# Kernel tuning notes

Measured on AMD Instinct MI355X. Metric: run time of the kernel, lower is better.

The kernel has to match this reference:

```python
import jax, jax.numpy as jnp
import numpy as np


def _icosa_group():
    """60 rotation matrices of the icosahedral rotation group (vertex anchors)."""
    phi = (1.0 + 5.0 ** 0.5) / 2.0

    def rot(axis, ang):
        a = np.asarray(axis, dtype=np.float64)
        a = a / np.linalg.norm(a)
        K = np.array([[0.0, -a[2], a[1]], [a[2], 0.0, -a[0]], [-a[1], a[0], 0.0]])
        return np.eye(3) + np.sin(ang) * K + (1.0 - np.cos(ang)) * (K @ K)

    # two distinct 5-fold vertex axes generate the full group of order 60
    gens = [rot([0.0, 1.0, phi], 2.0 * np.pi / 5.0),
            rot([0.0, -1.0, phi], 2.0 * np.pi / 5.0)]
    mats = {tuple(np.round(np.eye(3), 6).ravel()): np.eye(3)}
    frontier = [np.eye(3)]
    while frontier:
        new = []
        for m in frontier:
            for g in gens:
                p = g @ m
                k = tuple(np.round(p, 6).ravel())
                if k not in mats:
                    mats[k] = p
                    new.append(p)
        frontier = new
    Rs = np.stack([mats[k] for k in sorted(mats.keys())]).astype(np.float32)
    assert Rs.shape[0] == 60
    return Rs


def _normalize(x, axis=-1, eps=1e-12):
    n = jnp.linalg.norm(x, axis=axis, keepdims=True)
    return x / jnp.maximum(n, eps)


def setup_inputs() -> dict:
    key = jax.random.key(0)
    ks = jax.random.split(key, 6)
    bs, P, N = 2, 1024, 16
    d_in, d_out, K = 64, 32, 7
    neighbor_index = jax.random.randint(ks[0], (bs, P, N), 0, P, dtype=jnp.int32)
    vertices = jax.random.normal(ks[1], (bs, P, 3), dtype=jnp.float32)
    feature_map = jax.random.normal(ks[2], (bs, d_in, P, 3), dtype=jnp.float32)
    W = jax.random.normal(ks[3], (d_out, d_in, K, 3), dtype=jnp.float32) * (2.0 / (d_in * K * 3 + d_out * K * 3)) ** 0.5
    W_center = jax.random.normal(ks[4], (d_out, d_in), dtype=jnp.float32) * (2.0 / (d_in + d_out)) ** 0.5
    directions = jax.random.normal(ks[5], (d_out, K, 3), dtype=jnp.float32) * (2.0 / (d_out * 3 + K * 3)) ** 0.5
    Rs = jnp.asarray(_icosa_group())
    return {"neighbor_index": neighbor_index, "vertices": vertices,
            "feature_map": feature_map, "W": W, "W_center": W_center,
            "directions": directions, "Rs": Rs}


def reference(neighbor_index, vertices, feature_map, W, W_center, directions, Rs):
    bs, P, N = neighbor_index.shape
    d_out, d_in, K, _ = W.shape
    n_bin = 5
    interval = Rs.shape[0] // n_bin

    # neighbor direction unit vectors [b,p,n,3]
    nbrs = jax.vmap(lambda v_b, i_b: v_b[i_b])(vertices, neighbor_index)
    ndn = _normalize(nbrs - vertices[:, :, None, :])
    kd = _normalize(directions)  # [d,k,3]

    # ---- stage 1: rotation search (fully detached in the torch original) ----
    ndn_s = jax.lax.stop_gradient(ndn)
    kd_s = jax.lax.stop_gradient(kd)
    W_s = jax.lax.stop_gradient(W)
    fm_s = jax.lax.stop_gradient(feature_map)
    Rs_s = jax.lax.stop_gradient(Rs)

    r_vals, r_idxs = [], []
    for i in range(n_bin):
        Rsi = Rs_s[i * interval:(i + 1) * interval]  # [r,3,3]
        kd_ro = jnp.einsum('dkj,rij->dkir', kd_s, Rsi)          # [d,k,3,r]
        theta = jnp.einsum('dkjr,bpnj->bdkpnr', kd_ro, ndn_s)   # [b,d,k,p,n,r]
        W_ro = jnp.einsum('dckj,rij->dckir', W_s, Rsi)          # [d,c,k,3,r]
        fo = jnp.einsum('dckir,bcpi->bdkpr', W_ro, fm_s)        # [b,d,k,p,r]
        gathered = jax.vmap(lambda f_b, i_b: f_b[:, :, i_b, :])(fo, neighbor_index)  # [b,d,k,p,n,r]
        ka = gathered * theta
        ka = jnp.max(ka, axis=4)   # max over neighbors -> [b,d,k,p,r]
        ka = jnp.sum(ka, axis=2)   # sum over kernel pts -> [b,d,p,r]
        r_vals.append(jnp.max(ka, axis=-1))
        r_idxs.append(jnp.argmax(ka, axis=-1) + i * interval)
    r_vals = jnp.stack(r_vals, axis=-1)  # [b,d,p,5]
    r_idxs = jnp.stack(r_idxs, axis=-1)  # [b,d,p,5]
    best_bin = jnp.argmax(r_vals, axis=-1)  # [b,d,p]
    r_index = jnp.take_along_axis(r_idxs, best_bin[..., None], axis=-1)[..., 0]  # [b,d,p]
    match_R = Rs[r_index]  # [b,d,p,3,3]

    # ---- stage 2: apply best rotation (differentiable) ----
    kd_ro2 = jnp.einsum('dkj,bdpij->bdkpi', kd, match_R)               # [b,d,k,p,3]
    theta2 = jax.nn.relu(jnp.einsum('bdkpj,bpnj->bdkpn', kd_ro2, ndn))  # [b,d,k,p,n]
    fo2 = jnp.einsum('dckj,bdpij,bcpi->bdkp', W, match_R, feature_map)  # [b,d,k,p]
    gathered2 = jax.vmap(lambda f_b, i_b: f_b[:, :, i_b])(fo2, neighbor_index)  # [b,d,k,p,n]
    ka2 = gathered2 * theta2
    kaw2 = jnp.max(ka2, axis=4)  # [b,d,k,p]
    out = jnp.einsum('bdkp,bdkpi->bdpi', kaw2, kd_ro2)
    center = jnp.einsum('dc,bcpi->bdpi', W_center, feature_map)
    return out + center
```

## Files before the change

kernel.cpp:

```cpp
#include <hip/hip_runtime.h>
#include <math.h>

#define BS   2
#define PP   1024
#define NN   16
#define CIN  64
#define DOUT 32
#define KK   7
#define NR   60
#define NT2  30

#define OFF_NDN  0
#define OFF_KROT 98304
#define OFF_M    138624
#define OFF_PVAL 4332928
#define OFF_PIDX 6299008
#define OFF_FO2  6790528
#define OFF_RIDX 7314816

#define NEG_INF (-3.402823466e38f)

typedef float v2f __attribute__((ext_vector_type(2)));
typedef float v4f __attribute__((ext_vector_type(4)));

__device__ __forceinline__ float sload(const float* __restrict__ p, int idx) {
    return __int_as_float(__builtin_amdgcn_readfirstlane(__float_as_int(p[idx])));
}

__device__ __forceinline__ v2f pk_mul_sv(v2f s, v2f v) {
    v2f d; asm("v_pk_mul_f32 %0, %1, %2" : "=v"(d) : "s"(s), "v"(v)); return d;
}
__device__ __forceinline__ v2f pk_fma_svv(v2f s, v2f v, v2f c) {
    v2f d; asm("v_pk_fma_f32 %0, %1, %2, %3" : "=v"(d) : "s"(s), "v"(v), "v"(c)); return d;
}
__device__ __forceinline__ v2f pk_mul_vv(v2f a, v2f b) {
    v2f d; asm("v_pk_mul_f32 %0, %1, %2" : "=v"(d) : "v"(a), "v"(b)); return d;
}

__device__ __forceinline__ float quad_max(float x) {
    float y = __int_as_float(__builtin_amdgcn_mov_dpp(
        __float_as_int(x), 0xB1, 0xF, 0xF, true));
    x = fmaxf(x, y);
    float z = __int_as_float(__builtin_amdgcn_mov_dpp(
        __float_as_int(x), 0x4E, 0xF, 0xF, true));
    return fmaxf(x, z);
}

__global__ __launch_bounds__(256) void k_pre(const int* __restrict__ nbr,
                                             const float* __restrict__ vert,
                                             const float* __restrict__ dirs,
                                             const float* __restrict__ Rs,
                                             float* __restrict__ ws) {
    int tid = blockIdx.x * 256 + threadIdx.x;
    if (tid < BS * PP * NN) {
        int p = (tid >> 4) & (PP - 1);
        int b = tid >> 14;
        int q = nbr[tid];
        const float* vp = vert + ((b << 10) + p) * 3;
        const float* vq = vert + ((b << 10) + q) * 3;
        float dx = vq[0] - vp[0], dy = vq[1] - vp[1], dz = vq[2] - vp[2];
        float nrm = sqrtf(dx * dx + dy * dy + dz * dz);
        float den = fmaxf(nrm, 1e-12f);
        dx /= den; dy /= den; dz /= den;
        float* o = ws + OFF_NDN + tid * 3;
        o[0] = dx; o[1] = dy; o[2] = dz;
    }
    int t2 = tid - BS * PP * NN;
    if (t2 >= 0 && t2 < DOUT * NR * KK) {
        int k = t2 % KK;
        int r = (t2 / KK) % NR;
        int d = t2 / (KK * NR);
        const float* dk = dirs + (d * KK + k) * 3;
        float x = dk[0], y = dk[1], z = dk[2];
        float nrm = sqrtf(x * x + y * y + z * z);
        float den = fmaxf(nrm, 1e-12f);
        x /= den; y /= den; z /= den;
        const float* R = Rs + r * 9;
        float* o = ws + OFF_KROT + t2 * 3;
        o[0] = R[0] * x + R[1] * y + R[2] * z;
        o[1] = R[3] * x + R[4] * y + R[5] * z;
        o[2] = R[6] * x + R[7] * y + R[8] * z;
    }
}

__global__ __launch_bounds__(256, 2) void k_buildM(const float* __restrict__ fm,
                                                   const float* __restrict__ W,
                                                   float* __restrict__ Mout) {
    int d = blockIdx.y, b = blockIdx.z;
    int p = blockIdx.x * 256 + threadIdx.x;

    float M[64];
#pragma unroll
    for (int t = 0; t < 64; t++) M[t] = 0.f;

    const float* fbase = fm + (size_t)(b * CIN * PP + p) * 3;
    const float* wbase = W + (size_t)d * CIN * KK * 3;
    for (int c = 0; c < CIN; c++) {
        const float* f = fbase + c * PP * 3;
        float f0 = f[0], f1 = f[1], f2 = f[2];
        const float* wl = wbase + c * 21;
#pragma unroll
        for (int k = 0; k < KK; k++) {
#pragma unroll
            for (int j = 0; j < 3; j++) {
                float w = sload(wl, k * 3 + j);
                M[k * 9 + 0 + j] += w * f0;
                M[k * 9 + 3 + j] += w * f1;
                M[k * 9 + 6 + j] += w * f2;
            }
        }
    }
    float4* o = (float4*)(Mout + (size_t)(((b * DOUT + d) << 10) + p) * 64);
#pragma unroll
    for (int t = 0; t < 15; t++)
        o[t] = make_float4(M[4 * t], M[4 * t + 1], M[4 * t + 2], M[4 * t + 3]);
    o[15] = make_float4(M[60], M[61], M[62], 0.f);
}

__device__ __forceinline__ int fo_base(int p) {
    return (p << 2) ^ ((p >> 1) & 7);
}

__global__ __launch_bounds__(1024)
void k_score(const int* __restrict__ nbr,
             const float* __restrict__ Rs,
             const float* __restrict__ Mptr,
             const float* __restrict__ ndn,
             const float* __restrict__ krot,
             float* __restrict__ pval,
             unsigned char* __restrict__ pidx8) {
    __shared__ v4f fo4s[PP * 4];
    const int tile = blockIdx.x, d = blockIdx.y, b = blockIdx.z;
    const int bd = b * DOUT + d;
    const int rbase = tile * 2;
    const int tq = threadIdx.x >> 2;
    const int ns = threadIdx.x & 3;

    {
        const int p = threadIdx.x;
        float Rc0[9], Rc1[9];
#pragma unroll
        for (int j = 0; j < 9; j++) {
            Rc0[j] = sload(Rs, (rbase + 0) * 9 + j);
            Rc1[j] = sload(Rs, (rbase + 1) * 9 + j);
        }
        float fo0[KK], fo1[KK];
#pragma unroll
        for (int k = 0; k < KK; k++) { fo0[k] = 0.f; fo1[k] = 0.f; }

        const float4* m4 = (const float4*)(Mptr + (size_t)((bd << 10) + p) * 64);
#pragma unroll
        for (int t = 0; t < 16; t++) {
            float4 v = m4[t];
            float e[4] = {v.x, v.y, v.z, v.w};
#pragma unroll
            for (int ee = 0; ee < 4; ee++) {
                const int g = 4 * t + ee;
                if (g < 63) {
                    const int k = g / 9, r9 = g % 9;
                    fo0[k] += Rc0[r9] * e[ee];
                    fo1[k] += Rc1[r9] * e[ee];
                }
            }
            if ((t & 3) == 3)
                __builtin_amdgcn_sched_barrier(0);
        }
        const int fb = fo_base(p);
        v4f s0; s0.x = fo0[0]; s0.y = fo1[0]; s0.z = fo0[1]; s0.w = fo1[1];
        v4f s1; s1.x = fo0[2]; s1.y = fo1[2]; s1.z = fo0[3]; s1.w = fo1[3];
        v4f s2; s2.x = fo0[4]; s2.y = fo1[4]; s2.z = fo0[5]; s2.w = fo1[5];
        v4f s3; s3.x = fo0[6]; s3.y = fo1[6]; s3.z = 0.f;    s3.w = 0.f;
        fo4s[fb]     = s0;
        fo4s[fb ^ 1] = s1;
        fo4s[fb ^ 2] = s2;
        fo4s[fb ^ 3] = s3;
    }
    __syncthreads();

    v2f vkp[KK][3];
    {
        const int kb0 = (d * NR + rbase + 0) * 21;
        const int kb1 = (d * NR + rbase + 1) * 21;
#pragma unroll
        for (int k = 0; k < KK; k++)
#pragma unroll
            for (int c = 0; c < 3; c++) {
                v2f t; t.x = sload(krot, kb0 + k * 3 + c);
                       t.y = sload(krot, kb1 + k * 3 + c);
                vkp[k][c] = t;
            }
    }
    const v2f* fo2s = (const v2f*)fo4s;

#pragma unroll
    for (int pp = 0; pp < 4; pp++) {
        const int p2 = (pp << 8) + tq;

        int4 nv = *(const int4*)(nbr + (((size_t)((b << 10) + p2)) << 4) + (ns << 2));
        float u[12];
        {
            const float4* u4 = (const float4*)(ndn + ((size_t)((b << 10) + p2) * 16 + (ns << 2)) * 3);
            float4 a = u4[0], bb = u4[1], cc = u4[2];
            u[0] = a.x;  u[1] = a.y;  u[2] = a.z;  u[3] = a.w;
            u[4] = bb.x; u[5] = bb.y; u[6] = bb.z; u[7] = bb.w;
            u[8] = cc.x; u[9] = cc.y; u[10] = cc.z; u[11] = cc.w;
        }

        float mk0[KK], mk1[KK];
#pragma unroll
        for (int k = 0; k < KK; k++) { mk0[k] = NEG_INF; mk1[k] = NEG_INF; }

        int c0 = fo_base(nv.x);
        v4f A = fo4s[c0];
        v4f B = fo4s[c0 ^ 1];
        v4f C = fo4s[c0 ^ 2];
        v2f D = fo2s[(c0 ^ 3) << 1];

#pragma unroll
        for (int n = 0; n < 4; n++) {
            v4f An, Bn, Cn; v2f Dn;
            if (n < 3) {
                int qn = (n == 0) ? nv.y : (n == 1) ? nv.z : nv.w;
                int cn = fo_base(qn);
                An = fo4s[cn];
                Bn = fo4s[cn ^ 1];
                Cn = fo4s[cn ^ 2];
                Dn = fo2s[(cn ^ 3) << 1];
            }
            float u0 = u[n * 3], u1 = u[n * 3 + 1], u2 = u[n * 3 + 2];
            v2f u00; u00.x = u0; u00.y = u0;
            v2f u11; u11.x = u1; u11.y = u1;
            v2f u22; u22.x = u2; u22.y = u2;
#pragma unroll
            for (int k = 0; k < KK; k++) {
                v2f g;
                if (k == 0)      g = __builtin_shufflevector(A, A, 0, 1);
                else if (k == 1) g = __builtin_shufflevector(A, A, 2, 3);
                else if (k == 2) g = __builtin_shufflevector(B, B, 0, 1);
                else if (k == 3) g = __builtin_shufflevector(B, B, 2, 3);
                else if (k == 4) g = __builtin_shufflevector(C, C, 0, 1);
                else if (k == 5) g = __builtin_shufflevector(C, C, 2, 3);
                else             g = D;
                v2f t = pk_mul_sv(vkp[k][0], u00);
                t = pk_fma_svv(vkp[k][1], u11, t);
                t = pk_fma_svv(vkp[k][2], u22, t);
                v2f pr = pk_mul_vv(g, t);
                mk0[k] = fmaxf(mk0[k], pr.x);
                mk1[k] = fmaxf(mk1[k], pr.y);
            }
            if (n < 3) { A = An; B = Bn; C = Cn; D = Dn; }
        }
#pragma unroll
        for (int k = 0; k < KK; k++) {
            mk0[k] = quad_max(mk0[k]);
            mk1[k] = quad_max(mk1[k]);
        }
        float s0 = ((mk0[0] + mk0[1]) + (mk0[2] + mk0[3])) + ((mk0[4] + mk0[5]) + mk0[6]);
        float s1 = ((mk1[0] + mk1[1]) + (mk1[2] + mk1[3])) + ((mk1[4] + mk1[5]) + mk1[6]);
        float bl = s0; int bil = rbase;
        if (s1 > bl) { bl = s1; bil = rbase + 1; }

        if (ns == 0) {
            int pi = (bd * NT2 + tile) * PP + p2;
            pval[pi] = bl;
            pidx8[pi] = (unsigned char)bil;
        }
    }
}

__global__ __launch_bounds__(256, 2) void k_reduce(const float* __restrict__ Rs,
                                                   float* __restrict__ ws) {
    int gid = blockIdx.x * 256 + threadIdx.x;
    int bd = gid >> 10;
    int p = gid & (PP - 1);
    const unsigned char* pidx8 = (const unsigned char*)(ws + OFF_PIDX);
    float best = NEG_INF;
    int bi = 0;
    for (int t = 0; t < NT2; t++) {
        float v = ws[OFF_PVAL + (bd * NT2 + t) * PP + p];
        int idx = pidx8[(bd * NT2 + t) * PP + p];
        if (v > best) { best = v; bi = idx; }
    }
    ((int*)ws)[OFF_RIDX + gid] = bi;

    const float* R = Rs + bi * 9;
    float R0 = R[0], R1 = R[1], R2 = R[2];
    float R3 = R[3], R4 = R[4], R5 = R[5];
    float R6 = R[6], R7 = R[7], R8 = R[8];

    float M[64];
    const float4* m4 = (const float4*)(ws + OFF_M + (size_t)gid * 64);
#pragma unroll
    for (int t = 0; t < 16; t++) {
        float4 v = m4[t];
        M[4 * t] = v.x; M[4 * t + 1] = v.y; M[4 * t + 2] = v.z; M[4 * t + 3] = v.w;
    }
    float* o = ws + OFF_FO2 + (size_t)gid * 8;
#pragma unroll
    for (int k = 0; k < KK; k++) {
        o[k] = R0 * M[k * 9 + 0] + R1 * M[k * 9 + 1] + R2 * M[k * 9 + 2]
             + R3 * M[k * 9 + 3] + R4 * M[k * 9 + 4] + R5 * M[k * 9 + 5]
             + R6 * M[k * 9 + 6] + R7 * M[k * 9 + 7] + R8 * M[k * 9 + 8];
    }
    o[7] = 0.f;
}

__global__ __launch_bounds__(256, 2) void k_final(const int* __restrict__ nbr,
                                                  const float* __restrict__ fm,
                                                  const float* __restrict__ Wc,
                                                  const float* __restrict__ ws,
                                                  float* __restrict__ out) {
    __shared__ float fo2_s[PP * 8];
    __shared__ float krot_s[NR * KK * 3];
    int d = blockIdx.y, b = blockIdx.z;
    int bd = b * DOUT + d;
    for (int i = threadIdx.x; i < PP * 8; i += 256)
        fo2_s[i] = ws[OFF_FO2 + (size_t)bd * PP * 8 + i];
    for (int i = threadIdx.x; i < NR * KK * 3; i += 256)
        krot_s[i] = ws[OFF_KROT + d * NR * KK * 3 + i];
    __syncthreads();

    int p = blockIdx.x * 256 + threadIdx.x;
    int gid = (bd << 10) + p;
    int ri = ((const int*)ws)[OFF_RIDX + gid];

    float v[21];
#pragma unroll
    for (int t = 0; t < 21; t++) v[t] = krot_s[ri * 21 + t];

    float u[48];
    {
        const float4* u4 = (const float4*)(ws + OFF_NDN + (size_t)((b << 10) + p) * 48);
#pragma unroll
        for (int t = 0; t < 12; t++) {
            float4 w = u4[t];
            u[4 * t] = w.x; u[4 * t + 1] = w.y; u[4 * t + 2] = w.z; u[4 * t + 3] = w.w;
        }
    }
    int nidx[16];
    {
        const int4* n4 = (const int4*)(nbr + (size_t)((b << 10) + p) * 16);
#pragma unroll
        for (int t = 0; t < 4; t++) {
            int4 w = n4[t];
            nidx[4 * t] = w.x; nidx[4 * t + 1] = w.y; nidx[4 * t + 2] = w.z; nidx[4 * t + 3] = w.w;
        }
    }

    float kaw[7];
#pragma unroll
    for (int k = 0; k < KK; k++) kaw[k] = NEG_INF;
#pragma unroll
    for (int n = 0; n < NN; n++) {
        int q = nidx[n];
        const float4* fq = (const float4*)&fo2_s[q * 8];
        float4 a = fq[0], c4 = fq[1];
        float g[7] = {a.x, a.y, a.z, a.w, c4.x, c4.y, c4.z};
        float u0 = u[n * 3], u1 = u[n * 3 + 1], u2 = u[n * 3 + 2];
#pragma unroll
        for (int k = 0; k < KK; k++) {
            float th = fmaxf(v[k * 3] * u0 + v[k * 3 + 1] * u1 + v[k * 3 + 2] * u2, 0.f);
            kaw[k] = fmaxf(kaw[k], g[k] * th);
        }
    }
    float o0 = 0.f, o1 = 0.f, o2 = 0.f;
#pragma unroll
    for (int k = 0; k < KK; k++) {
        o0 += kaw[k] * v[k * 3];
        o1 += kaw[k] * v[k * 3 + 1];
        o2 += kaw[k] * v[k * 3 + 2];
    }
    const float* fbase = fm + (size_t)(b * CIN * PP + p) * 3;
    const float* wrow = Wc + d * CIN;
    for (int c = 0; c < CIN; c++) {
        float wcv = sload(wrow, c);
        const float* f = fbase + c * PP * 3;
        o0 += wcv * f[0];
        o1 += wcv * f[1];
        o2 += wcv * f[2];
    }
    out[(size_t)gid * 3 + 0] = o0;
    out[(size_t)gid * 3 + 1] = o1;
    out[(size_t)gid * 3 + 2] = o2;
}

extern "C" void kernel_launch(void* const* d_in, const int* in_sizes, int n_in,
                              void* d_out, int out_size, void* d_ws, size_t ws_size,
                              hipStream_t stream) {
    const int*   nbr  = (const int*)d_in[0];
    const float* vert = (const float*)d_in[1];
    const float* fm   = (const float*)d_in[2];
    const float* W    = (const float*)d_in[3];
    const float* Wc   = (const float*)d_in[4];
    const float* dirs = (const float*)d_in[5];
    const float* Rs   = (const float*)d_in[6];
    float* ws  = (float*)d_ws;
    float* out = (float*)d_out;

    k_pre<<<181, 256, 0, stream>>>(nbr, vert, dirs, Rs, ws);
    k_buildM<<<dim3(PP / 256, DOUT, BS), 256, 0, stream>>>(fm, W, ws + OFF_M);
    k_score<<<dim3(NT2, DOUT, BS), 1024, 0, stream>>>(
        nbr, Rs, ws + OFF_M, ws + OFF_NDN, ws + OFF_KROT,
        ws + OFF_PVAL, (unsigned char*)(ws + OFF_PIDX));
    k_reduce<<<dim3(BS * DOUT * PP / 256), 256, 0, stream>>>(Rs, ws);
    k_final<<<dim3(PP / 256, DOUT, BS), 256, 0, stream>>>(nbr, fm, Wc, ws, out);
}
```

Measured before the change: 183.7 us.

## Score one rotation per block and reduce argmax via packed 64-bit atomicMax

k_score now handles a single rotation per block (60 blocks in x, 512 threads) and stores only that rotation's 7 fo values per point in shared memory, halving LDS use. Rather than writing per-tile partial maxima and indices for k_reduce to scan, each point pushes an order-preserving float key packed with the rotation index into a 64-bit word through atomicMax. A small zeroing kernel is added. The aim is to remove the partial-result traffic and the 30-step reduction scan, at the cost of global atomic contention and losing the packed two-rotation math per thread.

Measured after the change: 221.9 us. +20.8%, slower.

```diff
diff --git a/kernel.cpp b/kernel.cpp
--- a/kernel.cpp
+++ b/kernel.cpp
@@ -8,15 +8,13 @@
 #define DOUT 32
 #define KK   7
 #define NR   60
-#define NT2  30
 
 #define OFF_NDN  0
 #define OFF_KROT 98304
 #define OFF_M    138624
-#define OFF_PVAL 4332928
-#define OFF_PIDX 6299008
-#define OFF_FO2  6790528
-#define OFF_RIDX 7314816
+#define OFF_PCK  4332928
+#define OFF_FO2  4464000
+#define OFF_RIDX 4988288
 
 #define NEG_INF (-3.402823466e38f)
 
@@ -44,6 +42,12 @@
     float z = __int_as_float(__builtin_amdgcn_mov_dpp(
         __float_as_int(x), 0x4E, 0xF, 0xF, true));
     return fmaxf(x, z);
+}
+
+__global__ __launch_bounds__(512) void k_zero(unsigned long long* __restrict__ pck) {
+    int i = blockIdx.x * 512 + threadIdx.x;
+    pck[i] = 0ull;
+    pck[i + 32768] = 0ull;
 }
 
 __global__ __launch_bounds__(256) void k_pre(const int* __restrict__ nbr,
@@ -117,84 +121,77 @@
     o[15] = make_float4(M[60], M[61], M[62], 0.f);
 }
 
-__device__ __forceinline__ int fo_base(int p) {
-    return (p << 2) ^ ((p >> 1) & 7);
-}
-
-__global__ __launch_bounds__(1024)
+__device__ __forceinline__ int fo_s0(int p) {
+    return (p << 1) ^ ((p >> 2) & 7);
+}
+
+__global__ __launch_bounds__(512)
 void k_score(const int* __restrict__ nbr,
              const float* __restrict__ Rs,
              const float* __restrict__ Mptr,
              const float* __restrict__ ndn,
              const float* __restrict__ krot,
-             float* __restrict__ pval,
-             unsigned char* __restrict__ pidx8) {
-    __shared__ v4f fo4s[PP * 4];
-    const int tile = blockIdx.x, d = blockIdx.y, b = blockIdx.z;
+             unsigned long long* __restrict__ pck) {
+    __shared__ v4f fo4s[2 * PP];
+    const int r = blockIdx.x, d = blockIdx.y, b = blockIdx.z;
     const int bd = b * DOUT + d;
-    const int rbase = tile * 2;
     const int tq = threadIdx.x >> 2;
     const int ns = threadIdx.x & 3;
 
     {
-        const int p = threadIdx.x;
-        float Rc0[9], Rc1[9];
-#pragma unroll
-        for (int j = 0; j < 9; j++) {
-            Rc0[j] = sload(Rs, (rbase + 0) * 9 + j);
-            Rc1[j] = sload(Rs, (rbase + 1) * 9 + j);
-        }
-        float fo0[KK], fo1[KK];
-#pragma unroll
-        for (int k = 0; k < KK; k++) { fo0[k] = 0.f; fo1[k] = 0.f; }
-
-        const float4* m4 = (const float4*)(Mptr + (size_t)((bd << 10) + p) * 64);
-#pragma unroll
-        for (int t = 0; t < 16; t++) {
-            float4 v = m4[t];
-            float e[4] = {v.x, v.y, v.z, v.w};
-#pragma unroll
-            for (int ee = 0; ee < 4; ee++) {
-                const int g = 4 * t + ee;
-                if (g < 63) {
-                    const int k = g / 9, r9 = g % 9;
-                    fo0[k] += Rc0[r9] * e[ee];
-                    fo1[k] += Rc1[r9] * e[ee];
+        float Rc[9];
+#pragma unroll
+        for (int j = 0; j < 9; j++) Rc[j] = sload(Rs, r * 9 + j);
+
+#pragma unroll
+        for (int half = 0; half < 2; half++) {
+            const int p = (half << 9) | threadIdx.x;
+            float fo[KK];
+#pragma unroll
+            for (int k = 0; k < KK; k++) fo[k] = 0.f;
+
+            const float4* m4 = (const float4*)(Mptr + (size_t)((bd << 10) + p) * 64);
+#pragma unroll
+            for (int t = 0; t < 16; t++) {
+                float4 v = m4[t];
+                float e[4] = {v.x, v.y, v.z, v.w};
+#pragma unroll
+                for (int ee = 0; ee < 4; ee++) {
+                    const int g = 4 * t + ee;
+                    if (g < 63) {
+                        const int k = g / 9, r9 = g % 9;
+                        fo[k] += Rc[r9] * e[ee];
+                    }
                 }
+                if ((t & 3) == 3)
+                    __builtin_amdgcn_sched_barrier(0);
             }
-            if ((t & 3) == 3)
-                __builtin_amdgcn_sched_barrier(0);
-        }
-        const int fb = fo_base(p);
-        v4f s0; s0.x = fo0[0]; s0.y = fo1[0]; s0.z = fo0[1]; s0.w = fo1[1];
-        v4f s1; s1.x = fo0[2]; s1.y = fo1[2]; s1.z = fo0[3]; s1.w = fo1[3];
-        v4f s2; s2.x = fo0[4]; s2.y = fo1[4]; s2.z = fo0[5]; s2.w = fo1[5];
-        v4f s3; s3.x = fo0[6]; s3.y = fo1[6]; s3.z = 0.f;    s3.w = 0.f;
-        fo4s[fb]     = s0;
-        fo4s[fb ^ 1] = s1;
-        fo4s[fb ^ 2] = s2;
-        fo4s[fb ^ 3] = s3;
+            const int s0 = fo_s0(p);
+            v4f a; a.x = fo[0]; a.y = fo[1]; a.z = fo[2]; a.w = fo[3];
+            v4f c; c.x = fo[4]; c.y = fo[5]; c.z = fo[6]; c.w = 0.f;
+            fo4s[s0]     = a;
+            fo4s[s0 ^ 1] = c;
+        }
     }
     __syncthreads();
 
-    v2f vkp[KK][3];
+    v2f vk01[3], vk23[3], vk45[3];
+    float vk6[3];
     {
-        const int kb0 = (d * NR + rbase + 0) * 21;
-        const int kb1 = (d * NR + rbase + 1) * 21;
-#pragma unroll
-        for (int k = 0; k < KK; k++)
-#pragma unroll
-            for (int c = 0; c < 3; c++) {
-                v2f t; t.x = sload(krot, kb0 + k * 3 + c);
-                       t.y = sload(krot, kb1 + k * 3 + c);
-                vkp[k][c] = t;
-            }
-    }
-    const v2f* fo2s = (const v2f*)fo4s;
-
-#pragma unroll
-    for (int pp = 0; pp < 4; pp++) {
-        const int p2 = (pp << 8) + tq;
+        const int kb = (d * NR + r) * 21;
+#pragma unroll
+        for (int c = 0; c < 3; c++) {
+            v2f t0; t0.x = sload(krot, kb + 0 * 3 + c); t0.y = sload(krot, kb + 1 * 3 + c);
+            v2f t1; t1.x = sload(krot, kb + 2 * 3 + c); t1.y = sload(krot, kb + 3 * 3 + c);
+            v2f t2; t2.x = sload(krot, kb + 4 * 3 + c); t2.y = sload(krot, kb + 5 * 3 + c);
+            vk01[c] = t0; vk23[c] = t1; vk45[c] = t2;
+            vk6[c] = sload(krot, kb + 6 * 3 + c);
+        }
+    }
+
+#pragma unroll 1
+    for (int pass = 0; pass < 8; pass++) {
+        const int p2 = (pass << 7) + tq;
 
         int4 nv = *(const int4*)(nbr + (((size_t)((b << 10) + p2)) << 4) + (ns << 2));
         float u[12];
@@ -206,64 +203,70 @@
             u[8] = cc.x; u[9] = cc.y; u[10] = cc.z; u[11] = cc.w;
         }
 
-        float mk0[KK], mk1[KK];
-#pragma unroll
-        for (int k = 0; k < KK; k++) { mk0[k] = NEG_INF; mk1[k] = NEG_INF; }
-
-        int c0 = fo_base(nv.x);
+        float mk[KK];
+#pragma unroll
+        for (int k = 0; k < KK; k++) mk[k] = NEG_INF;
+
+        int c0 = fo_s0(nv.x);
         v4f A = fo4s[c0];
         v4f B = fo4s[c0 ^ 1];
-        v4f C = fo4s[c0 ^ 2];
-        v2f D = fo2s[(c0 ^ 3) << 1];
 
 #pragma unroll
         for (int n = 0; n < 4; n++) {
-            v4f An, Bn, Cn; v2f Dn;
+            v4f An, Bn;
             if (n < 3) {
                 int qn = (n == 0) ? nv.y : (n == 1) ? nv.z : nv.w;
-                int cn = fo_base(qn);
+                int cn = fo_s0(qn);
                 An = fo4s[cn];
                 Bn = fo4s[cn ^ 1];
-                Cn = fo4s[cn ^ 2];
-                Dn = fo2s[(cn ^ 3) << 1];
             }
             float u0 = u[n * 3], u1 = u[n * 3 + 1], u2 = u[n * 3 + 2];
             v2f u00; u00.x = u0; u00.y = u0;
             v2f u11; u11.x = u1; u11.y = u1;
             v2f u22; u22.x = u2; u22.y = u2;
-#pragma unroll
-            for (int k = 0; k < KK; k++) {
-                v2f g;
-                if (k == 0)      g = __builtin_shufflevector(A, A, 0, 1);
-                else if (k == 1) g = __builtin_shufflevector(A, A, 2, 3);
-                else if (k == 2) g = __builtin_shufflevector(B, B, 0, 1);
-                else if (k == 3) g = __builtin_shufflevector(B, B, 2, 3);
-                else if (k == 4) g = __builtin_shufflevector(C, C, 0, 1);
-                else if (k == 5) g = __builtin_shufflevector(C, C, 2, 3);
-                else             g = D;
-                v2f t = pk_mul_sv(vkp[k][0], u00);
-                t = pk_fma_svv(vkp[k][1], u11, t);
-                t = pk_fma_svv(vkp[k][2], u22, t);
-                v2f pr = pk_mul_vv(g, t);
-                mk0[k] = fmaxf(mk0[k], pr.x);
-                mk1[k] = fmaxf(mk1[k], pr.y);
-            }
-            if (n < 3) { A = An; B = Bn; C = Cn; D = Dn; }
-        }
-#pragma unroll
-        for (int k = 0; k < KK; k++) {
-            mk0[k] = quad_max(mk0[k]);
-            mk1[k] = quad_max(mk1[k]);
-        }
-        float s0 = ((mk0[0] + mk0[1]) + (mk0[2] + mk0[3])) + ((mk0[4] + mk0[5]) + mk0[6]);
-        float s1 = ((mk1[0] + mk1[1]) + (mk1[2] + mk1[3])) + ((mk1[4] + mk1[5]) + mk1[6]);
-        float bl = s0; int bil = rbase;
-        if (s1 > bl) { bl = s1; bil = rbase + 1; }
+
+            v2f th01 = pk_mul_sv(vk01[0], u00);
+            th01 = pk_fma_svv(vk01[1], u11, th01);
+            th01 = pk_fma_svv(vk01[2], u22, th01);
+            v2f th23 = pk_mul_sv(vk23[0], u00);
+            th23 = pk_fma_svv(vk23[1], u11, th23);
+            th23 = pk_fma_svv(vk23[2], u22, th23);
+            v2f th45 = pk_mul_sv(vk45[0], u00);
+            th45 = pk_fma_svv(vk45[1], u11, th45);
+            th45 = pk_fma_svv(vk45[2], u22, th45);
+            float th6 = vk6[0] * u0 + vk6[1] * u1 + vk6[2] * u2;
+
+            v2f g01 = __builtin_shufflevector(A, A, 0, 1);
+            v2f g23 = __builtin_shufflevector(A, A, 2, 3);
+            v2f g45 = __builtin_shufflevector(B, B, 0, 1);
+            float g6 = B.z;
+
+            v2f p01 = pk_mul_vv(g01, th01);
+            v2f p23 = pk_mul_vv(g23, th23);
+            v2f p45 = pk_mul_vv(g45, th45);
+            float p6 = g6 * th6;
+
+            mk[0] = fmaxf(mk[0], p01.x);
+            mk[1] = fmaxf(mk[1], p01.y);
+            mk[2] = fmaxf(mk[2], p23.x);
+            mk[3] = fmaxf(mk[3], p23.y);
+            mk[4] = fmaxf(mk[4], p45.x);
+            mk[5] = fmaxf(mk[5], p45.y);
+            mk[6] = fmaxf(mk[6], p6);
+
+            if (n < 3) { A = An; B = Bn; }
+        }
+#pragma unroll
+        for (int k = 0; k < KK; k++) mk[k] = quad_max(mk[k]);
+
+        float s = ((mk[0] + mk[1]) + (mk[2] + mk[3])) + ((mk[4] + mk[5]) + mk[6]);
 
         if (ns == 0) {
-            int pi = (bd * NT2 + tile) * PP + p2;
-            pval[pi] = bl;
-            pidx8[pi] = (unsigned char)bil;
+            unsigned mono = __float_as_uint(s);
+            mono = (mono & 0x80000000u) ? ~mono : (mono | 0x80000000u);
+            unsigned long long key =
+                ((unsigned long long)mono << 8) | (unsigned long long)(255 - r);
+            atomicMax(pck + ((bd << 10) + p2), key);
         }
     }
 }
@@ -271,16 +274,8 @@
 __global__ __launch_bounds__(256, 2) void k_reduce(const float* __restrict__ Rs,
                                                    float* __restrict__ ws) {
     int gid = blockIdx.x * 256 + threadIdx.x;
-    int bd = gid >> 10;
-    int p = gid & (PP - 1);
-    const unsigned char* pidx8 = (const unsigned char*)(ws + OFF_PIDX);
-    float best = NEG_INF;
-    int bi = 0;
-    for (int t = 0; t < NT2; t++) {
-        float v = ws[OFF_PVAL + (bd * NT2 + t) * PP + p];
-        int idx = pidx8[(bd * NT2 + t) * PP + p];
-        if (v > best) { best = v; bi = idx; }
-    }
+    unsigned long long key = ((const unsigned long long*)(ws + OFF_PCK))[gid];
+    int bi = 255 - (int)(key & 0xFFull);
     ((int*)ws)[OFF_RIDX + gid] = bi;
 
     const float* R = Rs + bi * 9;
@@ -397,11 +392,12 @@
     float* ws  = (float*)d_ws;
     float* out = (float*)d_out;
 
+    k_zero<<<64, 512, 0, stream>>>((unsigned long long*)(ws + OFF_PCK));
     k_pre<<<181, 256, 0, stream>>>(nbr, vert, dirs, Rs, ws);
     k_buildM<<<dim3(PP / 256, DOUT, BS), 256, 0, stream>>>(fm, W, ws + OFF_M);
-    k_score<<<dim3(NT2, DOUT, BS), 1024, 0, stream>>>(
+    k_score<<<dim3(NR, DOUT, BS), 512, 0, stream>>>(
         nbr, Rs, ws + OFF_M, ws + OFF_NDN, ws + OFF_KROT,
-        ws + OFF_PVAL, (unsigned char*)(ws + OFF_PIDX));
+        (unsigned long long*)(ws + OFF_PCK));
     k_reduce<<<dim3(BS * DOUT * PP / 256), 256, 0, stream>>>(Rs, ws);
     k_final<<<dim3(PP / 256, DOUT, BS), 256, 0, stream>>>(nbr, fm, Wc, ws, out);
 }
```
